# Optimization experiments

Hardware: AMD Instinct MI355X
Metric: run time of the kernel (lower is better)

The kernel has to match this reference:

```python
import jax, jax.numpy as jnp
import numpy as np

D = 192      # model dim (out_channels)
DIN = 384    # d_inner = 2*D
N = 16       # d_state
DTR = 12     # dt_rank = ceil(D/16)
K = 4        # depthwise conv kernel size
NB = 3       # total mamba blocks (2 stacked + 1 in downsample)


def setup_inputs() -> dict:
    key = jax.random.key(0)
    ks = jax.random.split(key, 8)
    rn = lambda k, shape, s: jax.random.normal(k, shape, jnp.float32) * s
    inp = {
        "x": jax.random.normal(ks[0], (2, 96, 56, 56), jnp.float32),
        "proj_w": rn(ks[1], (D, 96), 0.1),
        "proj_b": jnp.zeros((D,), jnp.float32),
        "bn_g": jnp.ones((D,), jnp.float32),
        "bn_b": jnp.zeros((D,), jnp.float32),
        "bn_mean": jnp.zeros((D,), jnp.float32),
        "bn_var": jnp.ones((D,), jnp.float32),
        "ln_g": jnp.ones((NB, D), jnp.float32),
        "ln_b": jnp.zeros((NB, D), jnp.float32),
        "Win": rn(ks[2], (NB, 2 * DIN, D), 0.05),
        "b_in": jnp.zeros((NB, 2 * DIN), jnp.float32),
        "conv_w": rn(ks[3], (NB, DIN, K), 0.2),
        "conv_b": jnp.zeros((NB, DIN), jnp.float32),
        "Wx": rn(ks[4], (NB, DTR + 2 * N, DIN), 0.05),
        "Wdt": rn(ks[5], (NB, DIN, DTR), 0.05),
        "bdt": jnp.full((NB, DIN), -4.6, jnp.float32),  # softplus ~ 0.01
        "A_log": jnp.log(jnp.broadcast_to(jnp.arange(1, N + 1, dtype=jnp.float32), (NB, DIN, N))),
        "Dskip": jnp.ones((NB, DIN), jnp.float32),
        "Wout": rn(ks[6], (NB, D, DIN), 0.05),
        "bout": jnp.zeros((NB, D), jnp.float32),
    }
    return inp


def _mamba(x, ln_g, ln_b, Win, b_in, conv_w, conv_b, Wx, Wdt, bdt, A_log, Dskip, Wout, bout):
    # x: (B, C, H, W) -> flatten spatial dims to a sequence (B, L, C)
    B, C, H, W = x.shape
    L = H * W
    seq = x.reshape(B, C, L).transpose(0, 2, 1)
    mu = seq.mean(-1, keepdims=True)
    var = seq.var(-1, keepdims=True)
    h = (seq - mu) * jax.lax.rsqrt(var + 1e-5) * ln_g + ln_b  # LayerNorm
    xz = jnp.einsum('bld,ed->ble', h, Win) + b_in              # (B, L, 2*DIN)
    xi, z = jnp.split(xz, 2, axis=-1)
    # depthwise causal conv1d along L
    xc = jnp.pad(xi.transpose(0, 2, 1), ((0, 0), (0, 0), (K - 1, 0)))
    xc = jax.lax.conv_general_dilated(xc, conv_w[:, None, :], (1,), 'VALID',
                                      feature_group_count=DIN) + conv_b[:, None]
    xi = jax.nn.silu(xc).transpose(0, 2, 1)                    # (B, L, DIN)
    proj = jnp.einsum('ble,pe->blp', xi, Wx)                   # (B, L, DTR+2N)
    dtl = proj[..., :DTR]
    Bm = proj[..., DTR:DTR + N]
    Cm = proj[..., DTR + N:]
    dt = jax.nn.softplus(jnp.einsum('blr,er->ble', dtl, Wdt) + bdt)  # (B, L, DIN)
    A = -jnp.exp(A_log)                                         # (DIN, N)
    dA = jnp.exp(dt[..., None] * A)                             # (B, L, DIN, N)
    dBx = (dt * xi)[..., None] * Bm[:, :, None, :]              # (B, L, DIN, N)

    def step(hc, t):
        dA_t, dBx_t, C_t = t
        hc = dA_t * hc + dBx_t                                  # (B, DIN, N)
        return hc, jnp.einsum('ben,bn->be', hc, C_t)

    h0 = jnp.zeros((B, DIN, N), x.dtype)
    _, ys = jax.lax.scan(step, h0, (dA.transpose(1, 0, 2, 3),
                                    dBx.transpose(1, 0, 2, 3),
                                    Cm.transpose(1, 0, 2)))
    y = ys.transpose(1, 0, 2) + Dskip * xi
    y = y * jax.nn.silu(z)
    out = jnp.einsum('ble,de->bld', y, Wout) + bout
    return out.transpose(0, 2, 1).reshape(B, C, H, W)


def _maxpool2(x):
    return jax.lax.reduce_window(x, -jnp.inf, jax.lax.max,
                                 (1, 1, 2, 2), (1, 1, 2, 2), 'VALID')


def reference(x, proj_w, proj_b, bn_g, bn_b, bn_mean, bn_var, ln_g, ln_b, Win, b_in,
              conv_w, conv_b, Wx, Wdt, bdt, A_log, Dskip, Wout, bout):
    # proj (conv1x1) + BatchNorm (eval-mode running stats)
    x = jnp.einsum('bchw,oc->bohw', x, proj_w) + proj_b[:, None, None]
    x = (x - bn_mean[:, None, None]) * jax.lax.rsqrt(bn_var[:, None, None] + 1e-5) \
        * bn_g[:, None, None] + bn_b[:, None, None]
    blk = lambda i, v: _mamba(v, ln_g[i], ln_b[i], Win[i], b_in[i], conv_w[i], conv_b[i],
                              Wx[i], Wdt[i], bdt[i], A_log[i], Dskip[i], Wout[i], bout[i])
    for i in range(2):  # residual mamba blocks
        x = x + blk(i, x)
    skip = x
    x = blk(2, _maxpool2(x))  # downsample: maxpool then mamba (no residual)
    return (x, skip)
```

## Files before the change

kernel.cpp:

```cpp
#include <hip/hip_runtime.h>

typedef __attribute__((ext_vector_type(8))) __bf16 bf16x8;
typedef __attribute__((ext_vector_type(4))) __bf16 bf16x4;
typedef __attribute__((ext_vector_type(4))) float f32x4;

#define DEV static __device__ __forceinline__

DEV float fast_rcp(float x) { return __builtin_amdgcn_rcpf(x); }
DEV float sigm(float x) { return fast_rcp(1.f + __expf(-x)); }
DEV float siluf(float x) { return x * sigm(x); }
DEV float softplusf(float x) { return x > 20.f ? x : __logf(1.f + __expf(x)); }


__global__ __launch_bounds__(256) void k_proj_wcvt(
    const float* __restrict__ x, const float* __restrict__ pw,
    const float* __restrict__ pb, const float* __restrict__ bng,
    const float* __restrict__ bnb, const float* __restrict__ bnm,
    const float* __restrict__ bnv, float* __restrict__ v,
    const float* __restrict__ Win, const float* __restrict__ Wout,
    const float* __restrict__ Wx, __bf16* __restrict__ Wb)
{
  constexpr int SAP = 104;
  __shared__ __bf16 As[64 * SAP];
  __shared__ __bf16 Ws[64 * SAP];
  const int tid = threadIdx.x;
  const int bid = blockIdx.x;

  if (bid >= 294) {
    const int idx = ((bid - 294) * 256 + tid) * 4;
    if (idx < 714240) {
      const float* src;
      if (idx < 442368) src = Win + idx;
      else if (idx < 663552) src = Wout + (idx - 442368);
      else src = Wx + (idx - 663552);
      const float4 tv = *(const float4*)src;
      bf16x4 o;
      o[0] = (__bf16)tv.x; o[1] = (__bf16)tv.y;
      o[2] = (__bf16)tv.z; o[3] = (__bf16)tv.w;
      *(bf16x4*)(Wb + idx) = o;
    }
    return;
  }

  const int r0 = (bid % 98) * 64;
  const int col0 = (bid / 98) * 64;
  const int b = r0 / 3136, l0 = r0 % 3136;
  const int lane = tid & 63, wv = tid >> 6;
  const int rh = wv >> 1, ch = wv & 1;
  const int lm = lane & 15, quad = lane >> 4;

#pragma unroll
  for (int it = 0; it < 6; ++it) {
    const int idx = tid + it * 256;
    const int c = idx >> 4, l4 = idx & 15;
    const float4 t = *(const float4*)(x + ((size_t)(b * 96 + c)) * 3136 + l0 + l4 * 4);
    As[(l4 * 4 + 0) * SAP + c] = (__bf16)t.x;
    As[(l4 * 4 + 1) * SAP + c] = (__bf16)t.y;
    As[(l4 * 4 + 2) * SAP + c] = (__bf16)t.z;
    As[(l4 * 4 + 3) * SAP + c] = (__bf16)t.w;
  }
#pragma unroll
  for (int it = 0; it < 6; ++it) {
    const int idx = tid + it * 256;
    const int wr = idx / 24, kc = (idx % 24) * 4;
    const float4 t = *(const float4*)(pw + (size_t)(col0 + wr) * 96 + kc);
    bf16x4 o;
    o[0] = (__bf16)t.x; o[1] = (__bf16)t.y; o[2] = (__bf16)t.z; o[3] = (__bf16)t.w;
    *(bf16x4*)(&Ws[wr * SAP + kc]) = o;
  }
  __syncthreads();

  f32x4 acc[2][2] = {};
#pragma unroll
  for (int ks = 0; ks < 3; ++ks) {
    const int kb = ks * 32 + quad * 8;
    bf16x8 a0 = *(const bf16x8*)(&As[(rh * 32 + lm) * SAP + kb]);
    bf16x8 a1 = *(const bf16x8*)(&As[(rh * 32 + 16 + lm) * SAP + kb]);
    bf16x8 b0 = *(const bf16x8*)(&Ws[(ch * 32 + lm) * SAP + kb]);
    bf16x8 b1 = *(const bf16x8*)(&Ws[(ch * 32 + 16 + lm) * SAP + kb]);
    acc[0][0] = __builtin_amdgcn_mfma_f32_16x16x32_bf16(a0, b0, acc[0][0], 0, 0, 0);
    acc[0][1] = __builtin_amdgcn_mfma_f32_16x16x32_bf16(a0, b1, acc[0][1], 0, 0, 0);
    acc[1][0] = __builtin_amdgcn_mfma_f32_16x16x32_bf16(a1, b0, acc[1][0], 0, 0, 0);
    acc[1][1] = __builtin_amdgcn_mfma_f32_16x16x32_bf16(a1, b1, acc[1][1], 0, 0, 0);
  }

#pragma unroll
  for (int ti = 0; ti < 2; ++ti)
#pragma unroll
    for (int tj = 0; tj < 2; ++tj) {
      const int gcol = col0 + ch * 32 + tj * 16 + lm;
      const float s = rsqrtf(bnv[gcol] + 1e-5f) * bng[gcol];
      const float sh = (pb[gcol] - bnm[gcol]) * s + bnb[gcol];
#pragma unroll
      for (int j = 0; j < 4; ++j) {
        const int grow = r0 + rh * 32 + ti * 16 + quad * 4 + j;
        v[(size_t)grow * 192 + gcol] = acc[ti][tj][j] * s + sh;
      }
    }
}

__global__ __launch_bounds__(256) void k_conv(
    const float* __restrict__ xz, __bf16* __restrict__ xiB,
    const float* __restrict__ cw, const float* __restrict__ cb,
    int Lseq, int nthreads)
{
  const int idx = blockIdx.x * 256 + threadIdx.x;
  if (idx >= nthreads) return;
  const int e = idx % 384;
  const int seg = idx / 384;
  const int nseg = Lseq / 8;
  const int b = seg / nseg;
  const int l0 = (seg % nseg) * 8;
  const float4 w4 = *(const float4*)(cw + e * 4);
  const float bv = cb[e];
  float xv[11];
#pragma unroll
  for (int k = 0; k < 11; ++k) {
    const int l = l0 - 3 + k;
    xv[k] = (l >= 0) ? xz[(size_t)(b * Lseq + l) * 768 + e] : 0.f;
  }
#pragma unroll
  for (int j = 0; j < 8; ++j) {
    const float a = bv + xv[j] * w4.x + xv[j + 1] * w4.y + xv[j + 2] * w4.z + xv[j + 3] * w4.w;
    xiB[(size_t)(b * Lseq + l0 + j) * 384 + e] = (__bf16)siluf(a);
  }
}

template <int AMODE>
__global__ __launch_bounds__(256, 4) void k_gemm_xz(
    const float* __restrict__ A, const __bf16* __restrict__ W,
    const float* __restrict__ bias, float* __restrict__ O,
    int M, const float* __restrict__ lng, const float* __restrict__ lnb)
{
  constexpr int SA = 200;
  __shared__ __bf16 As[64 * SA];
  __shared__ float lnS[384];
  const int tid = threadIdx.x;
  const int r0 = blockIdx.x * 64;
  const int col0 = blockIdx.y * 128;
  const int lane = tid & 63, wv = tid >> 6;
  const int rh = wv & 1, ch = wv >> 1;
  const int lm = lane & 15, quad = lane >> 4;

  if (tid < 192) { lnS[tid] = lng[tid]; lnS[192 + tid] = lnb[tid]; }
  __syncthreads();

  {
    const int row = tid >> 2, part = tid & 3;
    const int gr = min(r0 + row, M - 1);
    const int cbase = part * 48;
    float4 tv[12];
    if constexpr (AMODE == 2) {
#pragma unroll
      for (int j = 0; j < 12; ++j)
        tv[j] = *(const float4*)(A + (size_t)gr * 192 + cbase + j * 4);
    } else {
      const int bb = gr / 784, l2 = gr % 784;
      const int h2 = l2 / 28, w2 = l2 % 28;
      const float* p0 = A + (size_t)(bb * 3136 + h2 * 112 + w2 * 2) * 192;
#pragma unroll
      for (int j = 0; j < 12; ++j) {
        const int cc = cbase + j * 4;
        const float4 a0 = *(const float4*)(p0 + cc);
        const float4 a1 = *(const float4*)(p0 + 192 + cc);
        const float4 a2 = *(const float4*)(p0 + 56 * 192 + cc);
        const float4 a3 = *(const float4*)(p0 + 57 * 192 + cc);
        tv[j].x = fmaxf(fmaxf(a0.x, a1.x), fmaxf(a2.x, a3.x));
        tv[j].y = fmaxf(fmaxf(a0.y, a1.y), fmaxf(a2.y, a3.y));
        tv[j].z = fmaxf(fmaxf(a0.z, a1.z), fmaxf(a2.z, a3.z));
        tv[j].w = fmaxf(fmaxf(a0.w, a1.w), fmaxf(a2.w, a3.w));
      }
    }
    float s = 0.f, sq = 0.f;
#pragma unroll
    for (int j = 0; j < 12; ++j) {
      s += tv[j].x + tv[j].y + tv[j].z + tv[j].w;
      sq += tv[j].x * tv[j].x + tv[j].y * tv[j].y + tv[j].z * tv[j].z + tv[j].w * tv[j].w;
    }
    s += __shfl_xor(s, 1); s += __shfl_xor(s, 2);
    sq += __shfl_xor(sq, 1); sq += __shfl_xor(sq, 2);
    const float mean = s * (1.f / 192.f);
    const float rstd = rsqrtf(sq * (1.f / 192.f) - mean * mean + 1e-5f);
#pragma unroll
    for (int j = 0; j < 12; ++j) {
      const int c = cbase + j * 4;
      bf16x4 o;
      o[0] = (__bf16)((tv[j].x - mean) * rstd * lnS[c + 0] + lnS[192 + c + 0]);
      o[1] = (__bf16)((tv[j].y - mean) * rstd * lnS[c + 1] + lnS[192 + c + 1]);
      o[2] = (__bf16)((tv[j].z - mean) * rstd * lnS[c + 2] + lnS[192 + c + 2]);
      o[3] = (__bf16)((tv[j].w - mean) * rstd * lnS[c + 3] + lnS[192 + c + 3]);
      *(bf16x4*)(&As[row * SA + c]) = o;
    }
  }
  __syncthreads();

  f32x4 acc[2][4] = {};
#pragma unroll
  for (int ks = 0; ks < 6; ++ks) {
    const int kb = ks * 32 + quad * 8;
    bf16x8 a0 = *(const bf16x8*)(&As[(rh * 32 + lm) * SA + kb]);
    bf16x8 a1 = *(const bf16x8*)(&As[(rh * 32 + 16 + lm) * SA + kb]);
#pragma unroll
    for (int tj = 0; tj < 4; ++tj) {
      const int gw = col0 + ch * 64 + tj * 16 + lm;
      bf16x8 bfr = *(const bf16x8*)(W + (size_t)gw * 192 + kb);
      acc[0][tj] = __builtin_amdgcn_mfma_f32_16x16x32_bf16(a0, bfr, acc[0][tj], 0, 0, 0);
      acc[1][tj] = __builtin_amdgcn_mfma_f32_16x16x32_bf16(a1, bfr, acc[1][tj], 0, 0, 0);
    }
  }

#pragma unroll
  for (int ti = 0; ti < 2; ++ti)
#pragma unroll
    for (int tj = 0; tj < 4; ++tj) {
      const int gcol = col0 + ch * 64 + tj * 16 + lm;
      const float bv = bias[gcol];
#pragma unroll
      for (int j = 0; j < 4; ++j) {
        const int rowt = rh * 32 + ti * 16 + quad * 4 + j;
        const int grow = r0 + rowt;
        if (grow < M) O[(size_t)grow * 768 + gcol] = acc[ti][tj][j] + bv;
      }
    }
}

constexpr int EPI_G2 = 1, EPI_RES = 2, EPI_RES_SKIP = 3, EPI_OUT2 = 4;

template <int EPI>
__global__ __launch_bounds__(256) void k_gemm(
    const __bf16* __restrict__ Ab, const __bf16* __restrict__ W,
    const float* __restrict__ bias, float* __restrict__ O,
    int M, int K, int Nvalid,
    float* __restrict__ dtlbuf, float* __restrict__ bcbuf,
    float* __restrict__ oflt)
{
  constexpr int SA = 200;
  __shared__ __bf16 As[64 * SA];
  __shared__ __bf16 Ws[64 * SA];
  const int tid = threadIdx.x;
  const int r0 = blockIdx.x * 64;
  const int col0 = blockIdx.y * 64;
  const int lane = tid & 63, wv = tid >> 6;
  const int rh = wv >> 1, ch = wv & 1;
  const int lm = lane & 15, quad = lane >> 4;

  f32x4 acc[2][2] = {};
  const int nkp = K / 192;
  for (int kp = 0; kp < nkp; ++kp) {
    if (kp) __syncthreads();
#pragma unroll
    for (int it = 0; it < 6; ++it) {
      const int idx = tid + it * 256;
      const int row = idx / 24, kc = (idx % 24) * 8;
      const int gr = min(r0 + row, M - 1);
      bf16x8 val = *(const bf16x8*)(Ab + (size_t)gr * K + kp * 192 + kc);
      *(bf16x8*)(&As[row * SA + kc]) = val;
    }
#pragma unroll
    for (int it = 0; it < 6; ++it) {
      const int idx = tid + it * 256;
      const int wr = idx / 24, kc = (idx % 24) * 8;
      const int gw = col0 + wr;
      bf16x8 val = {};
      if (gw < Nvalid) val = *(const bf16x8*)(W + (size_t)gw * K + kp * 192 + kc);
      *(bf16x8*)(&Ws[wr * SA + kc]) = val;
    }
    __syncthreads();
#pragma unroll
    for (int ks = 0; ks < 6; ++ks) {
      const int kb = ks * 32 + quad * 8;
      bf16x8 a0 = *(const bf16x8*)(&As[(rh * 32 + lm) * SA + kb]);
      bf16x8 a1 = *(const bf16x8*)(&As[(rh * 32 + 16 + lm) * SA + kb]);
#pragma unroll
      for (int tj = 0; tj < 2; ++tj) {
        bf16x8 bfr = *(const bf16x8*)(&Ws[(ch * 32 + tj * 16 + lm) * SA + kb]);
        acc[0][tj] = __builtin_amdgcn_mfma_f32_16x16x32_bf16(a0, bfr, acc[0][tj], 0, 0, 0);
        acc[1][tj] = __builtin_amdgcn_mfma_f32_16x16x32_bf16(a1, bfr, acc[1][tj], 0, 0, 0);
      }
    }
  }

  if constexpr (EPI == EPI_G2) {
    __shared__ float dtlS[64 * 12];
#pragma unroll
    for (int ti = 0; ti < 2; ++ti)
#pragma unroll
      for (int tj = 0; tj < 2; ++tj) {
        const int colt = ch * 32 + tj * 16 + lm;
#pragma unroll
        for (int j = 0; j < 4; ++j) {
          const int rowt = rh * 32 + ti * 16 + quad * 4 + j;
          const int grow = r0 + rowt;
          const float val = acc[ti][tj][j];
          if (colt < 12) dtlS[rowt * 12 + colt] = val;
          else if (colt < 44 && grow < M)
            bcbuf[(size_t)grow * 32 + (colt - 12)] = val;
        }
      }
    __syncthreads();
    for (int idx = tid; idx < 64 * 12; idx += 256) {
      const int grow = r0 + idx / 12;
      if (grow < M) dtlbuf[(size_t)grow * 12 + idx % 12] = dtlS[idx];
    }
  } else {
#pragma unroll
    for (int ti = 0; ti < 2; ++ti)
#pragma unroll
      for (int tj = 0; tj < 2; ++tj) {
        const int colt = ch * 32 + tj * 16 + lm;
        const int gcol = col0 + colt;
        const float bv = bias[gcol];
#pragma unroll
        for (int j = 0; j < 4; ++j) {
          const int rowt = rh * 32 + ti * 16 + quad * 4 + j;
          const int grow = r0 + rowt;
          if (grow >= M) continue;
          const float val = acc[ti][tj][j] + bv;
          if constexpr (EPI == EPI_RES) {
            O[(size_t)grow * 192 + gcol] += val;
          } else if constexpr (EPI == EPI_RES_SKIP) {
            const float nv = O[(size_t)grow * 192 + gcol] + val;
            O[(size_t)grow * 192 + gcol] = nv;
            const int b = grow / 3136, l = grow % 3136;
            oflt[b * 602112 + gcol * 3136 + l] = nv;
          } else {
            const int b = grow / 784, l = grow % 784;
            oflt[b * 150528 + gcol * 784 + l] = val;
          }
        }
      }
  }
}

constexpr int SC_LC = 14, SC_T = 7, SC_TN = 2;

DEV void compute_dts(const float* __restrict__ dtl, const float* __restrict__ Wdt,
                     const float* __restrict__ bdt, int rowbase, int e, int t,
                     float* dtlS, float* wdtS)
{
  for (int idx = t; idx < SC_LC * 12; idx += 128)
    dtlS[idx] = dtl[(size_t)(rowbase + idx / 12) * 12 + idx % 12];
#pragma unroll
  for (int r = 0; r < 12; ++r) wdtS[r * 128 + t] = Wdt[(size_t)e * 12 + r];
}

__global__ __launch_bounds__(128) void k_scan1(
    const float* __restrict__ dtl, const __bf16* __restrict__ xi,
    const float* __restrict__ bc, const float* __restrict__ Wdt,
    const float* __restrict__ bdt, const float* __restrict__ A_log,
    float* __restrict__ DT, float* __restrict__ S, int Lseq, int NC)
{
  __shared__ float Bs[SC_LC * 16];
  __shared__ float dts[SC_LC * 128];
  __shared__ float dtlS[SC_LC * 12];
  __shared__ float wdtS[12 * 128];
  const int t = threadIdx.x;
  const int e = blockIdx.y * 128 + t;
  const int c = blockIdx.x % NC;
  const int b = blockIdx.x / NC;
  const int rowbase = b * Lseq + c * SC_LC;

  for (int idx = t; idx < SC_LC * 16; idx += 128) {
    const int l = idx >> 4, q = idx & 15;
    Bs[idx] = bc[(size_t)(rowbase + l) * 32 + q];
  }
  compute_dts(dtl, Wdt, bdt, rowbase, e, t, dtlS, wdtS);
  const float bdte = bdt[e];

  float An2[16];
  {
    const float4* a4 = (const float4*)(A_log + e * 16);
    float4 t0 = a4[0], t1 = a4[1], t2 = a4[2], t3 = a4[3];
    float tmp[16] = {t0.x, t0.y, t0.z, t0.w, t1.x, t1.y, t1.z, t1.w,
                     t2.x, t2.y, t2.z, t2.w, t3.x, t3.y, t3.z, t3.w};
#pragma unroll
    for (int n = 0; n < 16; ++n) An2[n] = -__expf(tmp[n]) * 1.44269504f;
  }
  __syncthreads();
  float dtsum = 0.f;
  for (int l = 0; l < SC_LC; ++l) {
    float a = bdte;
#pragma unroll
    for (int r = 0; r < 12; ++r) a += dtlS[l * 12 + r] * wdtS[r * 128 + t];
    const float sp = softplusf(a);
    dts[l * 128 + t] = sp;
    dtsum += sp;
  }

  float h[16];
#pragma unroll
  for (int n = 0; n < 16; ++n) h[n] = 0.f;

  float xA[SC_T], xB[SC_T];
  auto LOADA = [&](int tt) {
#pragma unroll
    for (int j = 0; j < SC_T; ++j)
      xA[j] = (float)xi[(size_t)(rowbase + tt * SC_T + j) * 384 + e];
  };
  auto LOADB = [&](int tt) {
#pragma unroll
    for (int j = 0; j < SC_T; ++j)
      xB[j] = (float)xi[(size_t)(rowbase + tt * SC_T + j) * 384 + e];
  };
  auto COMP = [&](const float (&x8)[SC_T], int tt) {
#pragma unroll
    for (int j = 0; j < SC_T; ++j) {
      const int l = tt * SC_T + j;
      const float dtv = dts[l * 128 + t];
      const float u = dtv * x8[j];
      const float* Brow = &Bs[l * 16];
#pragma unroll
      for (int n = 0; n < 16; ++n) {
        const float a = __builtin_amdgcn_exp2f(dtv * An2[n]);
        h[n] = a * h[n] + u * Brow[n];
      }
    }
  };

  LOADA(0);
#pragma unroll
  for (int tt = 0; tt < SC_TN; ++tt) {
    if (tt & 1) { if (tt + 1 < SC_TN) LOADA(tt + 1); COMP(xB, tt); }
    else        { if (tt + 1 < SC_TN) LOADB(tt + 1); COMP(xA, tt); }
  }

  const size_t o = ((size_t)(b * NC + c) * 384 + e) * 16;
#pragma unroll
  for (int q = 0; q < 4; ++q)
    *(float4*)(S + o + q * 4) = make_float4(h[q*4], h[q*4+1], h[q*4+2], h[q*4+3]);
  DT[(size_t)(b * NC + c) * 384 + e] = dtsum;
}

__global__ __launch_bounds__(256) void k_carry(
    const float* __restrict__ DT, float* __restrict__ SH,
    const float* __restrict__ A_log, int NC)
{
  const int tid = blockIdx.x * 256 + threadIdx.x;
  const int b = tid / 6144, r = tid % 6144;
  const float An2 = -__expf(A_log[r]) * 1.44269504f;
  const size_t o = (size_t)b * NC * 6144 + r;
  const size_t od = (size_t)b * NC * 384 + (r >> 4);

  float sA[8], dA[8], sB[8], dB[8];
  auto LOAD = [&](float (&sv)[8], float (&dv)[8], int c0) {
#pragma unroll
    for (int k = 0; k < 8; ++k) {
      sv[k] = SH[o + (size_t)(c0 + k) * 6144];
      dv[k] = DT[od + (size_t)(c0 + k) * 384];
    }
  };
  float h = 0.f;
  auto COMP = [&](const float (&sv)[8], const float (&dv)[8], int c0) {
    float a[8];
#pragma unroll
    for (int k = 0; k < 8; ++k) a[k] = __builtin_amdgcn_exp2f(An2 * dv[k]);
#pragma unroll
    for (int k = 0; k < 8; ++k) {
      SH[o + (size_t)(c0 + k) * 6144] = h;
      h = a[k] * h + sv[k];
    }
  };

  LOAD(sA, dA, 0);
  for (int c0 = 0; c0 < NC; c0 += 16) {
    if (c0 + 8 < NC) LOAD(sB, dB, c0 + 8);
    COMP(sA, dA, c0);
    if (c0 + 8 < NC) {
      if (c0 + 16 < NC) LOAD(sA, dA, c0 + 16);
      COMP(sB, dB, c0 + 8);
    }
  }
}

__global__ __launch_bounds__(128) void k_scan2(
    const float* __restrict__ dtl, const __bf16* __restrict__ xi,
    const float* __restrict__ bc, const float* __restrict__ xz,
    const float* __restrict__ Wdt, const float* __restrict__ bdt,
    const float* __restrict__ A_log, const float* __restrict__ Dskip,
    const float* __restrict__ H0, __bf16* __restrict__ y, int Lseq, int NC)
{
  __shared__ float BCs[SC_LC * 32];
  __shared__ float dts[SC_LC * 128];
  __shared__ float dtlS[SC_LC * 12];
  __shared__ float wdtS[12 * 128];
  const int t = threadIdx.x;
  const int e = blockIdx.y * 128 + t;
  const int c = blockIdx.x % NC;
  const int b = blockIdx.x / NC;
  const int rowbase = b * Lseq + c * SC_LC;

  for (int idx = t; idx < SC_LC * 32; idx += 128)
    BCs[idx] = bc[(size_t)rowbase * 32 + idx];
  compute_dts(dtl, Wdt, bdt, rowbase, e, t, dtlS, wdtS);
  const float bdte = bdt[e];

  float An2[16];
  {
    const float4* a4 = (const float4*)(A_log + e * 16);
    float4 t0 = a4[0], t1 = a4[1], t2 = a4[2], t3 = a4[3];
    float tmp[16] = {t0.x, t0.y, t0.z, t0.w, t1.x, t1.y, t1.z, t1.w,
                     t2.x, t2.y, t2.z, t2.w, t3.x, t3.y, t3.z, t3.w};
#pragma unroll
    for (int n = 0; n < 16; ++n) An2[n] = -__expf(tmp[n]) * 1.44269504f;
  }
  float h[16];
  {
    const size_t o = ((size_t)(b * NC + c) * 384 + e) * 16;
    const float4* h4 = (const float4*)(H0 + o);
    float4 t0 = h4[0], t1 = h4[1], t2 = h4[2], t3 = h4[3];
    h[0]=t0.x; h[1]=t0.y; h[2]=t0.z; h[3]=t0.w;
    h[4]=t1.x; h[5]=t1.y; h[6]=t1.z; h[7]=t1.w;
    h[8]=t2.x; h[9]=t2.y; h[10]=t2.z; h[11]=t2.w;
    h[12]=t3.x; h[13]=t3.y; h[14]=t3.z; h[15]=t3.w;
  }
  __syncthreads();
  for (int l = 0; l < SC_LC; ++l) {
    float a = bdte;
#pragma unroll
    for (int r = 0; r < 12; ++r) a += dtlS[l * 12 + r] * wdtS[r * 128 + t];
    dts[l * 128 + t] = softplusf(a);
  }
  const float Dse = Dskip[e];

  float xA[SC_T], zA[SC_T], xB[SC_T], zB[SC_T];
  auto LOADA = [&](int tt) {
#pragma unroll
    for (int j = 0; j < SC_T; ++j) {
      const size_t r = (size_t)(rowbase + tt * SC_T + j);
      xA[j] = (float)xi[r * 384 + e];
      zA[j] = xz[r * 768 + 384 + e];
    }
  };
  auto LOADB = [&](int tt) {
#pragma unroll
    for (int j = 0; j < SC_T; ++j) {
      const size_t r = (size_t)(rowbase + tt * SC_T + j);
      xB[j] = (float)xi[r * 384 + e];
      zB[j] = xz[r * 768 + 384 + e];
    }
  };
  auto COMP = [&](const float (&x8)[SC_T], const float (&z8)[SC_T], int tt) {
#pragma unroll
    for (int j = 0; j < SC_T; ++j) {
      const int l = tt * SC_T + j;
      const float dtv = dts[l * 128 + t];
      const float xiv = x8[j];
      const float u = dtv * xiv;
      const float* Brow = &BCs[l * 32];
      const float* Crow = Brow + 16;
      float yv = 0.f;
#pragma unroll
      for (int n = 0; n < 16; ++n) {
        const float a = __builtin_amdgcn_exp2f(dtv * An2[n]);
        h[n] = a * h[n] + u * Brow[n];
        yv += h[n] * Crow[n];
      }
      y[(size_t)(rowbase + l) * 384 + e] = (__bf16)((yv + Dse * xiv) * siluf(z8[j]));
    }
  };

  LOADA(0);
#pragma unroll
  for (int tt = 0; tt < SC_TN; ++tt) {
    if (tt & 1) { if (tt + 1 < SC_TN) LOADA(tt + 1); COMP(xB, zB, tt); }
    else        { if (tt + 1 < SC_TN) LOADB(tt + 1); COMP(xA, zA, tt); }
  }
}

extern "C" void kernel_launch(void* const* d_in, const int* in_sizes, int n_in,
                              void* d_out, int out_size, void* d_ws, size_t ws_size,
                              hipStream_t stream)
{
  const float* x    = (const float*)d_in[0];
  const float* pw   = (const float*)d_in[1];
  const float* pb   = (const float*)d_in[2];
  const float* bng  = (const float*)d_in[3];
  const float* bnb  = (const float*)d_in[4];
  const float* bnm  = (const float*)d_in[5];
  const float* bnv  = (const float*)d_in[6];
  const float* lng  = (const float*)d_in[7];
  const float* lnb  = (const float*)d_in[8];
  const float* Win  = (const float*)d_in[9];
  const float* b_in = (const float*)d_in[10];
  const float* cw   = (const float*)d_in[11];
  const float* cb   = (const float*)d_in[12];
  const float* Wx   = (const float*)d_in[13];
  const float* Wdt  = (const float*)d_in[14];
  const float* bdt  = (const float*)d_in[15];
  const float* Alog = (const float*)d_in[16];
  const float* Dsk  = (const float*)d_in[17];
  const float* Wout = (const float*)d_in[18];
  const float* bout = (const float*)d_in[19];

  float* wsf = (float*)d_ws;
  float* v    = wsf;
  float* xz   = v + 1204224;
  float* dtlb = xz + 4816896;
  float* bcb  = dtlb + 75264;
  float* Sb   = bcb + 200704;
  float* Pb   = Sb + 2752512;
  __bf16* xiB = (__bf16*)(Pb + 2752512);
  __bf16* yB  = (__bf16*)(Pb + 2752512 + 1204224);
  __bf16* Wb  = (__bf16*)(Pb + 2752512 + 2408448);

  float* out0 = (float*)d_out;
  float* out1 = out0 + 301056;

  k_proj_wcvt<<<992, 256, 0, stream>>>(x, pw, pb, bng, bnb, bnm, bnv, v,
                                       Win, Wout, Wx, Wb);

  for (int i = 0; i < 3; ++i) {
    const int big = (i < 2) ? 1 : 0;
    const int Lseq = big ? 3136 : 784;
    const int M = 2 * Lseq;
    const int NC = Lseq / SC_LC;
    const int MB = (M + 63) / 64;
    const float* lng_i = lng + i * 192;
    const float* lnb_i = lnb + i * 192;
    const float* bin_i = b_in + i * 768;
    const float* cw_i  = cw + i * 384 * 4;
    const float* cb_i  = cb + i * 384;
    const float* Wdt_i = Wdt + i * 384 * 12;
    const float* bdt_i = bdt + i * 384;
    const float* Al_i  = Alog + i * 384 * 16;
    const float* Ds_i  = Dsk + i * 384;
    const float* bo_i  = bout + i * 192;
    const __bf16* Winb_i  = Wb + i * 147456;
    const __bf16* Woutb_i = Wb + 442368 + i * 73728;
    const __bf16* Wxb_i   = Wb + 663552 + i * 16896;

    if (big)
      k_gemm_xz<2><<<dim3(MB, 6), 256, 0, stream>>>(
          v, Winb_i, bin_i, xz, M, lng_i, lnb_i);
    else
      k_gemm_xz<3><<<dim3(MB, 6), 256, 0, stream>>>(
          v, Winb_i, bin_i, xz, M, lng_i, lnb_i);
    k_conv<<<(M * 384 / 8 + 255) / 256, 256, 0, stream>>>(
        xz, xiB, cw_i, cb_i, Lseq, M * 384 / 8);
    k_gemm<EPI_G2><<<dim3(MB, 1), 256, 0, stream>>>(
        xiB, Wxb_i, nullptr, nullptr, M, 384, 44, dtlb, bcb, nullptr);
    k_scan1<<<dim3(2 * NC, 3), 128, 0, stream>>>(
        dtlb, xiB, bcb, Wdt_i, bdt_i, Al_i, Pb, Sb, Lseq, NC);
    k_carry<<<48, 256, 0, stream>>>(Pb, Sb, Al_i, NC);
    k_scan2<<<dim3(2 * NC, 3), 128, 0, stream>>>(
        dtlb, xiB, bcb, xz, Wdt_i, bdt_i, Al_i, Ds_i, Sb, yB, Lseq, NC);
    if (i == 0)
      k_gemm<EPI_RES><<<dim3(MB, 3), 256, 0, stream>>>(
          yB, Woutb_i, bo_i, v, M, 384, 192, nullptr, nullptr, nullptr);
    else if (i == 1)
      k_gemm<EPI_RES_SKIP><<<dim3(MB, 3), 256, 0, stream>>>(
          yB, Woutb_i, bo_i, v, M, 384, 192, nullptr, nullptr, out1);
    else
      k_gemm<EPI_OUT2><<<dim3(MB, 3), 256, 0, stream>>>(
          yB, Woutb_i, bo_i, v, M, 384, 192, nullptr, nullptr, out0);
  }
}
```

Before: 354.6 us.

## Shrink GEMM row tile to 16 and read weights directly from global

The small-N GEMMs (x-projection and output projection) now use 16-row tiles instead of 64-row tiles, so each launch has four times as many blocks. Each wave computes one 16x16 output tile. Weight fragments are loaded straight from global memory into MFMA operands rather than staged in shared memory. The aim is better occupancy and lower LDS use across the GPU for these thin GEMMs, at the cost of more redundant weight loads, which rely on the cache, and less reuse per block.

```diff
diff --git a/kernel.cpp b/kernel.cpp
--- a/kernel.cpp
+++ b/kernel.cpp
@@ -227,7 +227,7 @@
 constexpr int EPI_G2 = 1, EPI_RES = 2, EPI_RES_SKIP = 3, EPI_OUT2 = 4;
 
 template <int EPI>
-__global__ __launch_bounds__(256) void k_gemm(
+__global__ __launch_bounds__(256) void k_gemm_s(
     const __bf16* __restrict__ Ab, const __bf16* __restrict__ W,
     const float* __restrict__ bias, float* __restrict__ O,
     int M, int K, int Nvalid,
@@ -235,100 +235,82 @@
     float* __restrict__ oflt)
 {
   constexpr int SA = 200;
-  __shared__ __bf16 As[64 * SA];
-  __shared__ __bf16 Ws[64 * SA];
+  __shared__ __bf16 As[16 * SA];
+  __shared__ float dtlS[(EPI == EPI_G2) ? 16 * 12 : 1];
   const int tid = threadIdx.x;
-  const int r0 = blockIdx.x * 64;
+  const int r0 = blockIdx.x * 16;
   const int col0 = blockIdx.y * 64;
   const int lane = tid & 63, wv = tid >> 6;
-  const int rh = wv >> 1, ch = wv & 1;
+  const int ch = wv;
   const int lm = lane & 15, quad = lane >> 4;
 
-  f32x4 acc[2][2] = {};
+  f32x4 acc = {};
   const int nkp = K / 192;
   for (int kp = 0; kp < nkp; ++kp) {
     if (kp) __syncthreads();
-#pragma unroll
-    for (int it = 0; it < 6; ++it) {
-      const int idx = tid + it * 256;
+    {
+      const int idx = tid;
       const int row = idx / 24, kc = (idx % 24) * 8;
       const int gr = min(r0 + row, M - 1);
-      bf16x8 val = *(const bf16x8*)(Ab + (size_t)gr * K + kp * 192 + kc);
-      *(bf16x8*)(&As[row * SA + kc]) = val;
-    }
-#pragma unroll
-    for (int it = 0; it < 6; ++it) {
-      const int idx = tid + it * 256;
-      const int wr = idx / 24, kc = (idx % 24) * 8;
-      const int gw = col0 + wr;
-      bf16x8 val = {};
-      if (gw < Nvalid) val = *(const bf16x8*)(W + (size_t)gw * K + kp * 192 + kc);
-      *(bf16x8*)(&Ws[wr * SA + kc]) = val;
+      if (row < 16)
+        *(bf16x8*)(&As[row * SA + kc]) =
+            *(const bf16x8*)(Ab + (size_t)gr * K + kp * 192 + kc);
+      const int idx2 = tid + 256;
+      if (idx2 < 384) {
+        const int row2 = idx2 / 24, kc2 = (idx2 % 24) * 8;
+        const int gr2 = min(r0 + row2, M - 1);
+        *(bf16x8*)(&As[row2 * SA + kc2]) =
+            *(const bf16x8*)(Ab + (size_t)gr2 * K + kp * 192 + kc2);
+      }
     }
     __syncthreads();
 #pragma unroll
     for (int ks = 0; ks < 6; ++ks) {
       const int kb = ks * 32 + quad * 8;
-      bf16x8 a0 = *(const bf16x8*)(&As[(rh * 32 + lm) * SA + kb]);
-      bf16x8 a1 = *(const bf16x8*)(&As[(rh * 32 + 16 + lm) * SA + kb]);
-#pragma unroll
-      for (int tj = 0; tj < 2; ++tj) {
-        bf16x8 bfr = *(const bf16x8*)(&Ws[(ch * 32 + tj * 16 + lm) * SA + kb]);
-        acc[0][tj] = __builtin_amdgcn_mfma_f32_16x16x32_bf16(a0, bfr, acc[0][tj], 0, 0, 0);
-        acc[1][tj] = __builtin_amdgcn_mfma_f32_16x16x32_bf16(a1, bfr, acc[1][tj], 0, 0, 0);
+      bf16x8 a0 = *(const bf16x8*)(&As[lm * SA + kb]);
+      const int gw = min(col0 + ch * 16 + lm, Nvalid - 1);
+      bf16x8 bfr = *(const bf16x8*)(W + (size_t)gw * K + kp * 192 + kb);
+      acc = __builtin_amdgcn_mfma_f32_16x16x32_bf16(a0, bfr, acc, 0, 0, 0);
+    }
+  }
+
+  const int colt = ch * 16 + lm;
+  if constexpr (EPI == EPI_G2) {
+#pragma unroll
+    for (int j = 0; j < 4; ++j) {
+      const int rowt = quad * 4 + j;
+      const int grow = r0 + rowt;
+      const float val = acc[j];
+      if (colt < 12) dtlS[rowt * 12 + colt] = val;
+      else if (colt < 44 && grow < M)
+        bcbuf[(size_t)grow * 32 + (colt - 12)] = val;
+    }
+    __syncthreads();
+    if (tid < 192) {
+      const int grow = r0 + tid / 12;
+      if (grow < M) dtlbuf[(size_t)grow * 12 + tid % 12] = dtlS[tid];
+    }
+  } else {
+    const int gcol = col0 + colt;
+    const float bv = bias[gcol];
+#pragma unroll
+    for (int j = 0; j < 4; ++j) {
+      const int rowt = quad * 4 + j;
+      const int grow = r0 + rowt;
+      if (grow >= M) continue;
+      const float val = acc[j] + bv;
+      if constexpr (EPI == EPI_RES) {
+        O[(size_t)grow * 192 + gcol] += val;
+      } else if constexpr (EPI == EPI_RES_SKIP) {
+        const float nv = O[(size_t)grow * 192 + gcol] + val;
+        O[(size_t)grow * 192 + gcol] = nv;
+        const int b = grow / 3136, l = grow % 3136;
+        oflt[b * 602112 + gcol * 3136 + l] = nv;
+      } else {
+        const int b = grow / 784, l = grow % 784;
+        oflt[b * 150528 + gcol * 784 + l] = val;
       }
     }
-  }
-
-  if constexpr (EPI == EPI_G2) {
-    __shared__ float dtlS[64 * 12];
-#pragma unroll
-    for (int ti = 0; ti < 2; ++ti)
-#pragma unroll
-      for (int tj = 0; tj < 2; ++tj) {
-        const int colt = ch * 32 + tj * 16 + lm;
-#pragma unroll
-        for (int j = 0; j < 4; ++j) {
-          const int rowt = rh * 32 + ti * 16 + quad * 4 + j;
-          const int grow = r0 + rowt;
-          const float val = acc[ti][tj][j];
-          if (colt < 12) dtlS[rowt * 12 + colt] = val;
-          else if (colt < 44 && grow < M)
-            bcbuf[(size_t)grow * 32 + (colt - 12)] = val;
-        }
-      }
-    __syncthreads();
-    for (int idx = tid; idx < 64 * 12; idx += 256) {
-      const int grow = r0 + idx / 12;
-      if (grow < M) dtlbuf[(size_t)grow * 12 + idx % 12] = dtlS[idx];
-    }
-  } else {
-#pragma unroll
-    for (int ti = 0; ti < 2; ++ti)
-#pragma unroll
-      for (int tj = 0; tj < 2; ++tj) {
-        const int colt = ch * 32 + tj * 16 + lm;
-        const int gcol = col0 + colt;
-        const float bv = bias[gcol];
-#pragma unroll
-        for (int j = 0; j < 4; ++j) {
-          const int rowt = rh * 32 + ti * 16 + quad * 4 + j;
-          const int grow = r0 + rowt;
-          if (grow >= M) continue;
-          const float val = acc[ti][tj][j] + bv;
-          if constexpr (EPI == EPI_RES) {
-            O[(size_t)grow * 192 + gcol] += val;
-          } else if constexpr (EPI == EPI_RES_SKIP) {
-            const float nv = O[(size_t)grow * 192 + gcol] + val;
-            O[(size_t)grow * 192 + gcol] = nv;
-            const int b = grow / 3136, l = grow % 3136;
-            oflt[b * 602112 + gcol * 3136 + l] = nv;
-          } else {
-            const int b = grow / 784, l = grow % 784;
-            oflt[b * 150528 + gcol * 784 + l] = val;
-          }
-        }
-      }
   }
 }
 
@@ -615,6 +597,7 @@
     const int M = 2 * Lseq;
     const int NC = Lseq / SC_LC;
     const int MB = (M + 63) / 64;
+    const int MB16 = M / 16;
     const float* lng_i = lng + i * 192;
     const float* lnb_i = lnb + i * 192;
     const float* bin_i = b_in + i * 768;
@@ -637,7 +620,7 @@
           v, Winb_i, bin_i, xz, M, lng_i, lnb_i);
     k_conv<<<(M * 384 / 8 + 255) / 256, 256, 0, stream>>>(
         xz, xiB, cw_i, cb_i, Lseq, M * 384 / 8);
-    k_gemm<EPI_G2><<<dim3(MB, 1), 256, 0, stream>>>(
+    k_gemm_s<EPI_G2><<<dim3(MB16, 1), 256, 0, stream>>>(
         xiB, Wxb_i, nullptr, nullptr, M, 384, 44, dtlb, bcb, nullptr);
     k_scan1<<<dim3(2 * NC, 3), 128, 0, stream>>>(
         dtlb, xiB, bcb, Wdt_i, bdt_i, Al_i, Pb, Sb, Lseq, NC);
@@ -645,13 +628,13 @@
     k_scan2<<<dim3(2 * NC, 3), 128, 0, stream>>>(
         dtlb, xiB, bcb, xz, Wdt_i, bdt_i, Al_i, Ds_i, Sb, yB, Lseq, NC);
     if (i == 0)
-      k_gemm<EPI_RES><<<dim3(MB, 3), 256, 0, stream>>>(
+      k_gemm_s<EPI_RES><<<dim3(MB16, 3), 256, 0, stream>>>(
           yB, Woutb_i, bo_i, v, M, 384, 192, nullptr, nullptr, nullptr);
     else if (i == 1)
-      k_gemm<EPI_RES_SKIP><<<dim3(MB, 3), 256, 0, stream>>>(
+      k_gemm_s<EPI_RES_SKIP><<<dim3(MB16, 3), 256, 0, stream>>>(
           yB, Woutb_i, bo_i, v, M, 384, 192, nullptr, nullptr, out1);
     else
-      k_gemm<EPI_OUT2><<<dim3(MB, 3), 256, 0, stream>>>(
+      k_gemm_s<EPI_OUT2><<<dim3(MB16, 3), 256, 0, stream>>>(
           yB, Woutb_i, bo_i, v, M, 384, 192, nullptr, nullptr, out0);
   }
 }
```

Measured after the change: 346.1 us. 2.4% less time.
